# Optimization experiments

Measured on AMD Instinct MI355X. Metric: run time of the kernel, lower is better.

Reference implementation:

```python
import jax, jax.numpy as jnp
import numpy as np

N, E, D, H, O = 10000, 640000, 128, 256, 1


def setup_inputs() -> dict:
    key = jax.random.key(0)
    ks = jax.random.split(key, 10)
    s = 0.05
    return {
        "x": jax.random.normal(ks[0], (N, D), dtype=jnp.float32),
        "edge_index": jax.random.randint(ks[1], (2, E), 0, N, dtype=jnp.int64),
        # GraphConv (PyG): lin_rel (with bias) applied to sum-aggregated neighbors,
        # lin_root (no bias) applied to self features.
        "W_rel": jax.random.normal(ks[2], (D, D), dtype=jnp.float32) * s,
        "b_rel": jnp.zeros((D,), dtype=jnp.float32),
        "W_root": jax.random.normal(ks[3], (D, D), dtype=jnp.float32) * s,
        # MLP: D -> H -> H -> O, ReLU between layers
        "W1": jax.random.normal(ks[4], (H, D), dtype=jnp.float32) * s,
        "b1": jnp.zeros((H,), dtype=jnp.float32),
        "W2": jax.random.normal(ks[5], (H, H), dtype=jnp.float32) * s,
        "b2": jnp.zeros((H,), dtype=jnp.float32),
        "W3": jax.random.normal(ks[6], (O, H), dtype=jnp.float32) * s,
        "b3": jnp.zeros((O,), dtype=jnp.float32),
    }


def reference(x, edge_index, W_rel, b_rel, W_root, W1, b1, W2, b2, W3, b3):
    src, dst = edge_index[0], edge_index[1]
    # gather source features along edges, scatter-add to destinations
    agg = jax.ops.segment_sum(x[src], dst, num_segments=N)  # [N, D]
    h = agg @ W_rel.T + b_rel + x @ W_root.T                 # GraphConv out [N, D]
    h = jax.nn.relu(h @ W1.T + b1)
    h = jax.nn.relu(h @ W2.T + b2)
    h = h @ W3.T + b3                                        # [N, O]
    return jax.nn.sigmoid(h)
```

## Files before the change

kernel.cpp:

```cpp
#include <hip/hip_runtime.h>
#include <hip/hip_bf16.h>
#include <cmath>

constexpr int N_NODES = 10000;
constexpr int D_IN = 128;
constexpr int H_DIM = 256;

constexpr int NB = 157;
constexpr int BCAP = 8192;
constexpr int EPB_A = 4096;

typedef unsigned short u16;
typedef short bf16x8 __attribute__((ext_vector_type(8)));
typedef float f32x4 __attribute__((ext_vector_type(4)));

__device__ inline u16 f2bf(float f) {
    return __builtin_bit_cast(u16, __float2bfloat16(f));
}
__device__ inline float bf2f(u16 u) {
    unsigned int v = (unsigned int)u << 16;
    return __builtin_bit_cast(float, v);
}

__global__ __launch_bounds__(256)
void binsort_a(const int* __restrict__ ei, int* __restrict__ gcnt,
               int* __restrict__ buckets, int E) {
    __shared__ int lcnt[NB], gbase[NB];
    const int t = threadIdx.x;
    for (int i = t; i < NB; i += 256) lcnt[i] = 0;
    __syncthreads();
    const int e0 = blockIdx.x * EPB_A + t;
    int packed[16], lpos[16], bb[16];
#pragma unroll
    for (int j = 0; j < 16; ++j) {
        int e = e0 + j * 256;
        if (e < E) {
            int s = ei[e], d = ei[E + e];
            int b = d >> 6;
            bb[j] = b;
            packed[j] = ((d & 63) << 16) | s;
            lpos[j] = atomicAdd(&lcnt[b], 1);
        } else bb[j] = -1;
    }
    __syncthreads();
    for (int i = t; i < NB; i += 256)
        gbase[i] = atomicAdd(&gcnt[i], lcnt[i]);
    __syncthreads();
#pragma unroll
    for (int j = 0; j < 16; ++j)
        if (bb[j] >= 0)
            buckets[bb[j] * BCAP + gbase[bb[j]] + lpos[j]] = packed[j];
}

__global__ __launch_bounds__(64)
void bucket_scan(const int* __restrict__ gcnt, int* __restrict__ bbase,
                 int* __restrict__ offsets) {
    const int t = threadIdx.x;
    int v[3], sum = 0;
#pragma unroll
    for (int j = 0; j < 3; ++j) {
        int idx = t * 3 + j;
        int d = (idx < NB) ? gcnt[idx] : 0;
        v[j] = sum;
        sum += d;
    }
    int incl = sum;
#pragma unroll
    for (int off = 1; off < 64; off <<= 1) {
        int o = __shfl_up(incl, off);
        if (t >= off) incl += o;
    }
    int excl = incl - sum;
#pragma unroll
    for (int j = 0; j < 3; ++j) {
        int idx = t * 3 + j;
        if (idx < NB) bbase[idx] = excl + v[j];
    }
    if (t == 63) offsets[N_NODES] = incl;
}

__global__ __launch_bounds__(256)
void binsort_b(const int* __restrict__ gcnt, const int* __restrict__ bbase,
               const int* __restrict__ buckets, int* __restrict__ sorted_src,
               int* __restrict__ offsets) {
    __shared__ int edges[BCAP];
    __shared__ int deg[64], cur[64];
    const int b = blockIdx.x, t = threadIdx.x;
    int cnt = gcnt[b]; if (cnt > BCAP) cnt = BCAP;
    const int base = bbase[b];
    if (t < 64) deg[t] = 0;
    __syncthreads();
    for (int i = t; i < cnt; i += 256) {
        int p = buckets[b * BCAP + i];
        edges[i] = p;
        atomicAdd(&deg[p >> 16], 1);
    }
    __syncthreads();
    if (t < 64) {
        int d = deg[t];
        int incl = d;
#pragma unroll
        for (int off = 1; off < 64; off <<= 1) {
            int o = __shfl_up(incl, off);
            if (t >= off) incl += o;
        }
        int excl = incl - d;
        cur[t] = excl;
        int node = b * 64 + t;
        if (node < N_NODES) offsets[node] = base + excl;
    }
    __syncthreads();
    for (int i = t; i < cnt; i += 256) {
        int p = edges[i];
        int pos = atomicAdd(&cur[p >> 16], 1);
        sorted_src[base + pos] = p & 0xffff;
    }
}

__global__ __launch_bounds__(256)
void gather_sum_kernel(const float* __restrict__ x,
                       const int* __restrict__ offsets,
                       const int* __restrict__ sorted_src,
                       u16* __restrict__ A0, int M) {
    int wid = (blockIdx.x * blockDim.x + threadIdx.x) >> 6;
    if (wid >= M) return;
    int lane = threadIdx.x & 63;
    int c = (lane & 31) * 4;
    int r = lane >> 5;
    int beg = offsets[wid], end = offsets[wid + 1];
    int half = (end - beg + 1) >> 1;
    int i = r ? beg + half : beg;
    const int i1 = r ? end : beg + half;
    float4 a0 = {0, 0, 0, 0}, a1 = {0, 0, 0, 0}, a2 = {0, 0, 0, 0}, a3 = {0, 0, 0, 0};
    for (; i + 4 <= i1; i += 4) {
        int s0 = sorted_src[i + 0], s1 = sorted_src[i + 1];
        int s2 = sorted_src[i + 2], s3 = sorted_src[i + 3];
        const float4 v0 = *reinterpret_cast<const float4*>(x + (size_t)s0 * D_IN + c);
        const float4 v1 = *reinterpret_cast<const float4*>(x + (size_t)s1 * D_IN + c);
        const float4 v2 = *reinterpret_cast<const float4*>(x + (size_t)s2 * D_IN + c);
        const float4 v3 = *reinterpret_cast<const float4*>(x + (size_t)s3 * D_IN + c);
        a0.x += v0.x; a0.y += v0.y; a0.z += v0.z; a0.w += v0.w;
        a1.x += v1.x; a1.y += v1.y; a1.z += v1.z; a1.w += v1.w;
        a2.x += v2.x; a2.y += v2.y; a2.z += v2.z; a2.w += v2.w;
        a3.x += v3.x; a3.y += v3.y; a3.z += v3.z; a3.w += v3.w;
    }
    for (; i < i1; ++i) {
        int s = sorted_src[i];
        const float4 v = *reinterpret_cast<const float4*>(x + (size_t)s * D_IN + c);
        a0.x += v.x; a0.y += v.y; a0.z += v.z; a0.w += v.w;
    }
    a0.x += a1.x + a2.x + a3.x;
    a0.y += a1.y + a2.y + a3.y;
    a0.z += a1.z + a2.z + a3.z;
    a0.w += a1.w + a2.w + a3.w;
    a0.x += __shfl_xor(a0.x, 32);
    a0.y += __shfl_xor(a0.y, 32);
    a0.z += __shfl_xor(a0.z, 32);
    a0.w += __shfl_xor(a0.w, 32);
    if (r == 0) {
        ushort4 o;
        o.x = f2bf(a0.x); o.y = f2bf(a0.y); o.z = f2bf(a0.z); o.w = f2bf(a0.w);
        *reinterpret_cast<ushort4*>(A0 + (size_t)wid * 256 + c) = o;
    }
}

__global__ __launch_bounds__(256)
void cast_x_kernel(const float* __restrict__ x, u16* __restrict__ A0, int total4) {
    int idx = blockIdx.x * blockDim.x + threadIdx.x;
    if (idx >= total4) return;
    int row = idx >> 5;
    int c = (idx & 31) * 4;
    float4 v = *reinterpret_cast<const float4*>(x + (size_t)row * D_IN + c);
    ushort4 o;
    o.x = f2bf(v.x); o.y = f2bf(v.y); o.z = f2bf(v.z); o.w = f2bf(v.w);
    *reinterpret_cast<ushort4*>(A0 + (size_t)row * 256 + 128 + c) = o;
}

__global__ __launch_bounds__(256)
void cast_w_kernel(const float* __restrict__ W_rel, const float* __restrict__ W_root,
                   const float* __restrict__ W1, const float* __restrict__ W2,
                   u16* __restrict__ Wcat, u16* __restrict__ W1b, u16* __restrict__ W2b) {
    int idx4 = (blockIdx.x * blockDim.x + threadIdx.x) * 4;
    const float* src;
    u16* dst;
    if (idx4 < 32768) {
        int n = idx4 >> 8, k = idx4 & 255;
        src = (k < 128) ? W_rel + n * 128 + k : W_root + n * 128 + (k - 128);
        dst = Wcat + idx4;
    } else if (idx4 < 65536) {
        src = W1 + (idx4 - 32768);
        dst = W1b + (idx4 - 32768);
    } else {
        src = W2 + (idx4 - 65536);
        dst = W2b + (idx4 - 65536);
    }
    float4 v = *reinterpret_cast<const float4*>(src);
    ushort4 o;
    o.x = f2bf(v.x); o.y = f2bf(v.y); o.z = f2bf(v.z); o.w = f2bf(v.w);
    *reinterpret_cast<ushort4*>(dst) = o;
}

template <int ACT>
__global__ __launch_bounds__(256)
void mfma_gemm(const u16* __restrict__ A, const u16* __restrict__ W,
               const float* __restrict__ bias, u16* __restrict__ C,
               int M, int N, int K) {
    constexpr int LDT = 80;
    __shared__ short As[64 * LDT];
    __shared__ short Ws[64 * LDT];
    const int t = threadIdx.x;
    const int m0 = blockIdx.y * 64;
    const int n0 = blockIdx.x * 64;
    const int w = t >> 6, lane = t & 63;
    const int wr = w >> 1, wc = w & 1;
    const int m_lane = lane & 15, q = lane >> 4;
    f32x4 acc[2][2] = {};
    for (int k0 = 0; k0 < K; k0 += 64) {
        __syncthreads();
#pragma unroll
        for (int L = 0; L < 2; ++L) {
            int idx = t + 256 * L;
            int row = idx >> 3;
            int kc = (idx & 7) * 8;
            int ar = m0 + row; if (ar >= M) ar = M - 1;
            bf16x8 av = *reinterpret_cast<const bf16x8*>(A + (size_t)ar * K + k0 + kc);
            bf16x8 wv = *reinterpret_cast<const bf16x8*>(W + (size_t)(n0 + row) * K + k0 + kc);
            *reinterpret_cast<bf16x8*>(&As[row * LDT + kc]) = av;
            *reinterpret_cast<bf16x8*>(&Ws[row * LDT + kc]) = wv;
        }
        __syncthreads();
#pragma unroll
        for (int kk = 0; kk < 64; kk += 32) {
            const int koff = kk + q * 8;
            bf16x8 af[2], bf[2];
#pragma unroll
            for (int i = 0; i < 2; ++i)
                af[i] = *reinterpret_cast<const bf16x8*>(
                    &As[(wr * 32 + i * 16 + m_lane) * LDT + koff]);
#pragma unroll
            for (int j = 0; j < 2; ++j)
                bf[j] = *reinterpret_cast<const bf16x8*>(
                    &Ws[(wc * 32 + j * 16 + m_lane) * LDT + koff]);
#pragma unroll
            for (int i = 0; i < 2; ++i)
#pragma unroll
                for (int j = 0; j < 2; ++j)
                    acc[i][j] = __builtin_amdgcn_mfma_f32_16x16x32_bf16(
                        af[i], bf[j], acc[i][j], 0, 0, 0);
        }
    }
#pragma unroll
    for (int i = 0; i < 2; ++i)
#pragma unroll
        for (int j = 0; j < 2; ++j) {
            int col = n0 + wc * 32 + j * 16 + m_lane;
            float b = bias[col];
#pragma unroll
            for (int r = 0; r < 4; ++r) {
                int row = m0 + wr * 32 + i * 16 + q * 4 + r;
                if (row >= M) continue;
                float v = acc[i][j][r] + b;
                if (ACT == 1) v = fmaxf(v, 0.f);
                C[(size_t)row * N + col] = f2bf(v);
            }
        }
}

__global__ __launch_bounds__(256)
void head_kernel(const u16* __restrict__ h2, const float* __restrict__ W3,
                 const float* __restrict__ b3, float* __restrict__ out, int M) {
    int wave = threadIdx.x >> 6;
    int lane = threadIdx.x & 63;
    int n = blockIdx.x * 4 + wave;
    if (n >= M) return;
    ushort4 hu = *reinterpret_cast<const ushort4*>(h2 + (size_t)n * H_DIM + lane * 4);
    float4 w = *reinterpret_cast<const float4*>(W3 + lane * 4);
    float dot = bf2f(hu.x) * w.x + bf2f(hu.y) * w.y + bf2f(hu.z) * w.z + bf2f(hu.w) * w.w;
#pragma unroll
    for (int off = 32; off > 0; off >>= 1) dot += __shfl_down(dot, off);
    if (lane == 0) {
        float v = dot + b3[0];
        out[n] = 1.0f / (1.0f + expf(-v));
    }
}

extern "C" void kernel_launch(void* const* d_in, const int* in_sizes, int n_in,
                              void* d_out, int out_size, void* d_ws, size_t ws_size,
                              hipStream_t stream) {
    const float* x      = (const float*)d_in[0];
    const int*   ei     = (const int*)d_in[1];
    const float* W_rel  = (const float*)d_in[2];
    const float* b_rel  = (const float*)d_in[3];
    const float* W_root = (const float*)d_in[4];
    const float* W1     = (const float*)d_in[5];
    const float* b1     = (const float*)d_in[6];
    const float* W2     = (const float*)d_in[7];
    const float* b2     = (const float*)d_in[8];
    const float* W3     = (const float*)d_in[9];
    const float* b3     = (const float*)d_in[10];
    float* out = (float*)d_out;
    const int E = in_sizes[1] / 2;

    char* p = (char*)d_ws;
    auto carve = [&](size_t bytes) { char* r = p; p += (bytes + 63) & ~size_t(63); return r; };
    u16* A0   = (u16*)carve((size_t)N_NODES * 256 * 2);
    u16* h0   = (u16*)carve((size_t)N_NODES * 128 * 2);
    u16* h1   = (u16*)carve((size_t)N_NODES * 256 * 2);
    u16* h2   = (u16*)carve((size_t)N_NODES * 256 * 2);
    u16* Wcat = (u16*)carve(128 * 256 * 2);
    u16* W1b  = (u16*)carve(256 * 128 * 2);
    u16* W2b  = (u16*)carve(256 * 256 * 2);
    int* offsets    = (int*)carve((N_NODES + 4) * 4);
    int* gcnt       = (int*)carve(NB * 4);
    int* bbase      = (int*)carve(NB * 4);
    int* buckets    = (int*)carve((size_t)NB * BCAP * 4);
    int* sorted_src = (int*)carve((size_t)E * 4);

    hipMemsetAsync(gcnt, 0, NB * sizeof(int), stream);
    binsort_a<<<(E + EPB_A - 1) / EPB_A, 256, 0, stream>>>(ei, gcnt, buckets, E);
    bucket_scan<<<1, 64, 0, stream>>>(gcnt, bbase, offsets);
    binsort_b<<<NB, 256, 0, stream>>>(gcnt, bbase, buckets, sorted_src, offsets);
    gather_sum_kernel<<<(N_NODES * 64 + 255) / 256, 256, 0, stream>>>(
        x, offsets, sorted_src, A0, N_NODES);
    cast_x_kernel<<<(N_NODES * 32 + 255) / 256, 256, 0, stream>>>(x, A0, N_NODES * 32);
    cast_w_kernel<<<131072 / 4 / 256, 256, 0, stream>>>(W_rel, W_root, W1, W2,
                                                        Wcat, W1b, W2b);
    {
        dim3 g(128 / 64, (N_NODES + 63) / 64);
        mfma_gemm<0><<<g, 256, 0, stream>>>(A0, Wcat, b_rel, h0, N_NODES, 128, 256);
    }
    {
        dim3 g(256 / 64, (N_NODES + 63) / 64);
        mfma_gemm<1><<<g, 256, 0, stream>>>(h0, W1b, b1, h1, N_NODES, 256, 128);
    }
    {
        dim3 g(256 / 64, (N_NODES + 63) / 64);
        mfma_gemm<1><<<g, 256, 0, stream>>>(h1, W2b, b2, h2, N_NODES, 256, 256);
    }
    head_kernel<<<(N_NODES + 3) / 4, 256, 0, stream>>>(h2, W3, b3, out, N_NODES);
}
```

Baseline: 155.1 us.

## Fuse MLP GEMMs and head into one kernel, merge prep and scan launches

Replaces the three separate MFMA GEMM launches and the head kernel with a single fused kernel that keeps each 64-row tile's intermediates in shared memory. It streams weights straight from global memory and folds the final W3 dot product and sigmoid into the epilogue. It also merges the x/weight casts and the gcnt zeroing into one prep kernel, and moves the bucket scan into binsort_b. The neighbor gather now reads a bf16 copy of x, halving gather bytes at a small precision cost. Together these cut launch count and intermediate global traffic, at the risk of lower occupancy from large shared memory and uncached weight reads.

```diff
diff --git a/kernel.cpp b/kernel.cpp
--- a/kernel.cpp
+++ b/kernel.cpp
@@ -20,6 +20,48 @@
 __device__ inline float bf2f(u16 u) {
     unsigned int v = (unsigned int)u << 16;
     return __builtin_bit_cast(float, v);
+}
+
+constexpr int PREP_XB = 1250, PREP_WB = 128;
+__global__ __launch_bounds__(256)
+void prep_kernel(const float* __restrict__ x,
+                 const float* __restrict__ W_rel, const float* __restrict__ W_root,
+                 const float* __restrict__ W1, const float* __restrict__ W2,
+                 u16* __restrict__ x_bf, u16* __restrict__ A0,
+                 u16* __restrict__ Wcat, u16* __restrict__ W1b, u16* __restrict__ W2b,
+                 int* __restrict__ gcnt) {
+    const int bid = blockIdx.x, t = threadIdx.x;
+    if (bid < PREP_XB) {
+        int idx = bid * 256 + t;
+        if (idx >= N_NODES * 32) return;
+        int row = idx >> 5, c = (idx & 31) * 4;
+        float4 v = *reinterpret_cast<const float4*>(x + (size_t)row * D_IN + c);
+        ushort4 o;
+        o.x = f2bf(v.x); o.y = f2bf(v.y); o.z = f2bf(v.z); o.w = f2bf(v.w);
+        *reinterpret_cast<ushort4*>(x_bf + (size_t)row * D_IN + c) = o;
+        *reinterpret_cast<ushort4*>(A0 + (size_t)row * 256 + 128 + c) = o;
+    } else if (bid < PREP_XB + PREP_WB) {
+        int idx4 = ((bid - PREP_XB) * 256 + t) * 4;
+        const float* src;
+        u16* dst;
+        if (idx4 < 32768) {
+            int n = idx4 >> 8, k = idx4 & 255;
+            src = (k < 128) ? W_rel + n * 128 + k : W_root + n * 128 + (k - 128);
+            dst = Wcat + idx4;
+        } else if (idx4 < 65536) {
+            src = W1 + (idx4 - 32768);
+            dst = W1b + (idx4 - 32768);
+        } else {
+            src = W2 + (idx4 - 65536);
+            dst = W2b + (idx4 - 65536);
+        }
+        float4 v = *reinterpret_cast<const float4*>(src);
+        ushort4 o;
+        o.x = f2bf(v.x); o.y = f2bf(v.y); o.z = f2bf(v.z); o.w = f2bf(v.w);
+        *reinterpret_cast<ushort4*>(dst) = o;
+    } else {
+        if (t < NB) gcnt[t] = 0;
+    }
 }
 
 __global__ __launch_bounds__(256)
@@ -52,44 +94,38 @@
             buckets[bb[j] * BCAP + gbase[bb[j]] + lpos[j]] = packed[j];
 }
 
-__global__ __launch_bounds__(64)
-void bucket_scan(const int* __restrict__ gcnt, int* __restrict__ bbase,
-                 int* __restrict__ offsets) {
-    const int t = threadIdx.x;
-    int v[3], sum = 0;
-#pragma unroll
-    for (int j = 0; j < 3; ++j) {
-        int idx = t * 3 + j;
-        int d = (idx < NB) ? gcnt[idx] : 0;
-        v[j] = sum;
-        sum += d;
-    }
-    int incl = sum;
-#pragma unroll
-    for (int off = 1; off < 64; off <<= 1) {
-        int o = __shfl_up(incl, off);
-        if (t >= off) incl += o;
-    }
-    int excl = incl - sum;
-#pragma unroll
-    for (int j = 0; j < 3; ++j) {
-        int idx = t * 3 + j;
-        if (idx < NB) bbase[idx] = excl + v[j];
-    }
-    if (t == 63) offsets[N_NODES] = incl;
-}
-
-__global__ __launch_bounds__(256)
-void binsort_b(const int* __restrict__ gcnt, const int* __restrict__ bbase,
-               const int* __restrict__ buckets, int* __restrict__ sorted_src,
-               int* __restrict__ offsets) {
+__global__ __launch_bounds__(256)
+void binsort_b(const int* __restrict__ gcnt, const int* __restrict__ buckets,
+               int* __restrict__ sorted_src, int* __restrict__ offsets, int E) {
     __shared__ int edges[BCAP];
     __shared__ int deg[64], cur[64];
+    __shared__ int sbase;
     const int b = blockIdx.x, t = threadIdx.x;
+    if (t < 64) {
+        int v[3], sum = 0;
+#pragma unroll
+        for (int j = 0; j < 3; ++j) {
+            int idx = t * 3 + j;
+            int d = (idx < NB) ? gcnt[idx] : 0;
+            v[j] = sum;
+            sum += d;
+        }
+        int incl = sum;
+#pragma unroll
+        for (int off = 1; off < 64; off <<= 1) {
+            int o = __shfl_up(incl, off);
+            if (t >= off) incl += o;
+        }
+        int excl = incl - sum;
+#pragma unroll
+        for (int j = 0; j < 3; ++j)
+            if (t * 3 + j == b) sbase = excl + v[j];
+    }
+    if (t < 64) deg[t] = 0;
+    if (b == 0 && t == 0) offsets[N_NODES] = E;
+    __syncthreads();
+    const int base = sbase;
     int cnt = gcnt[b]; if (cnt > BCAP) cnt = BCAP;
-    const int base = bbase[b];
-    if (t < 64) deg[t] = 0;
-    __syncthreads();
     for (int i = t; i < cnt; i += 256) {
         int p = buckets[b * BCAP + i];
         edges[i] = p;
@@ -118,7 +154,7 @@
 }
 
 __global__ __launch_bounds__(256)
-void gather_sum_kernel(const float* __restrict__ x,
+void gather_sum_kernel(const u16* __restrict__ x_bf,
                        const int* __restrict__ offsets,
                        const int* __restrict__ sorted_src,
                        u16* __restrict__ A0, int M) {
@@ -135,19 +171,19 @@
     for (; i + 4 <= i1; i += 4) {
         int s0 = sorted_src[i + 0], s1 = sorted_src[i + 1];
         int s2 = sorted_src[i + 2], s3 = sorted_src[i + 3];
-        const float4 v0 = *reinterpret_cast<const float4*>(x + (size_t)s0 * D_IN + c);
-        const float4 v1 = *reinterpret_cast<const float4*>(x + (size_t)s1 * D_IN + c);
-        const float4 v2 = *reinterpret_cast<const float4*>(x + (size_t)s2 * D_IN + c);
-        const float4 v3 = *reinterpret_cast<const float4*>(x + (size_t)s3 * D_IN + c);
-        a0.x += v0.x; a0.y += v0.y; a0.z += v0.z; a0.w += v0.w;
-        a1.x += v1.x; a1.y += v1.y; a1.z += v1.z; a1.w += v1.w;
-        a2.x += v2.x; a2.y += v2.y; a2.z += v2.z; a2.w += v2.w;
-        a3.x += v3.x; a3.y += v3.y; a3.z += v3.z; a3.w += v3.w;
+        ushort4 v0 = *reinterpret_cast<const ushort4*>(x_bf + (size_t)s0 * D_IN + c);
+        ushort4 v1 = *reinterpret_cast<const ushort4*>(x_bf + (size_t)s1 * D_IN + c);
+        ushort4 v2 = *reinterpret_cast<const ushort4*>(x_bf + (size_t)s2 * D_IN + c);
+        ushort4 v3 = *reinterpret_cast<const ushort4*>(x_bf + (size_t)s3 * D_IN + c);
+        a0.x += bf2f(v0.x); a0.y += bf2f(v0.y); a0.z += bf2f(v0.z); a0.w += bf2f(v0.w);
+        a1.x += bf2f(v1.x); a1.y += bf2f(v1.y); a1.z += bf2f(v1.z); a1.w += bf2f(v1.w);
+        a2.x += bf2f(v2.x); a2.y += bf2f(v2.y); a2.z += bf2f(v2.z); a2.w += bf2f(v2.w);
+        a3.x += bf2f(v3.x); a3.y += bf2f(v3.y); a3.z += bf2f(v3.z); a3.w += bf2f(v3.w);
     }
     for (; i < i1; ++i) {
         int s = sorted_src[i];
-        const float4 v = *reinterpret_cast<const float4*>(x + (size_t)s * D_IN + c);
-        a0.x += v.x; a0.y += v.y; a0.z += v.z; a0.w += v.w;
+        ushort4 v = *reinterpret_cast<const ushort4*>(x_bf + (size_t)s * D_IN + c);
+        a0.x += bf2f(v.x); a0.y += bf2f(v.y); a0.z += bf2f(v.z); a0.w += bf2f(v.w);
     }
     a0.x += a1.x + a2.x + a3.x;
     a0.y += a1.y + a2.y + a3.y;
@@ -165,122 +201,145 @@
 }
 
 __global__ __launch_bounds__(256)
-void cast_x_kernel(const float* __restrict__ x, u16* __restrict__ A0, int total4) {
-    int idx = blockIdx.x * blockDim.x + threadIdx.x;
-    if (idx >= total4) return;
-    int row = idx >> 5;
-    int c = (idx & 31) * 4;
-    float4 v = *reinterpret_cast<const float4*>(x + (size_t)row * D_IN + c);
-    ushort4 o;
-    o.x = f2bf(v.x); o.y = f2bf(v.y); o.z = f2bf(v.z); o.w = f2bf(v.w);
-    *reinterpret_cast<ushort4*>(A0 + (size_t)row * 256 + 128 + c) = o;
-}
-
-__global__ __launch_bounds__(256)
-void cast_w_kernel(const float* __restrict__ W_rel, const float* __restrict__ W_root,
-                   const float* __restrict__ W1, const float* __restrict__ W2,
-                   u16* __restrict__ Wcat, u16* __restrict__ W1b, u16* __restrict__ W2b) {
-    int idx4 = (blockIdx.x * blockDim.x + threadIdx.x) * 4;
-    const float* src;
-    u16* dst;
-    if (idx4 < 32768) {
-        int n = idx4 >> 8, k = idx4 & 255;
-        src = (k < 128) ? W_rel + n * 128 + k : W_root + n * 128 + (k - 128);
-        dst = Wcat + idx4;
-    } else if (idx4 < 65536) {
-        src = W1 + (idx4 - 32768);
-        dst = W1b + (idx4 - 32768);
-    } else {
-        src = W2 + (idx4 - 65536);
-        dst = W2b + (idx4 - 65536);
-    }
-    float4 v = *reinterpret_cast<const float4*>(src);
-    ushort4 o;
-    o.x = f2bf(v.x); o.y = f2bf(v.y); o.z = f2bf(v.z); o.w = f2bf(v.w);
-    *reinterpret_cast<ushort4*>(dst) = o;
-}
-
-template <int ACT>
-__global__ __launch_bounds__(256)
-void mfma_gemm(const u16* __restrict__ A, const u16* __restrict__ W,
-               const float* __restrict__ bias, u16* __restrict__ C,
-               int M, int N, int K) {
-    constexpr int LDT = 80;
-    __shared__ short As[64 * LDT];
-    __shared__ short Ws[64 * LDT];
-    const int t = threadIdx.x;
-    const int m0 = blockIdx.y * 64;
-    const int n0 = blockIdx.x * 64;
+void fused_mlp(const u16* __restrict__ A0, const u16* __restrict__ Wcat,
+               const u16* __restrict__ W1b, const u16* __restrict__ W2b,
+               const float* __restrict__ b_rel, const float* __restrict__ b1,
+               const float* __restrict__ b2, const float* __restrict__ W3,
+               const float* __restrict__ b3, float* __restrict__ out, int M) {
+    __shared__ u16 sm[25600];
+    __shared__ float part[64][2];
+    u16* bufA  = sm;
+    u16* bufH0 = sm + 16896;
+    const int t = threadIdx.x, b = blockIdx.x;
     const int w = t >> 6, lane = t & 63;
-    const int wr = w >> 1, wc = w & 1;
-    const int m_lane = lane & 15, q = lane >> 4;
-    f32x4 acc[2][2] = {};
-    for (int k0 = 0; k0 < K; k0 += 64) {
-        __syncthreads();
-#pragma unroll
-        for (int L = 0; L < 2; ++L) {
-            int idx = t + 256 * L;
-            int row = idx >> 3;
-            int kc = (idx & 7) * 8;
-            int ar = m0 + row; if (ar >= M) ar = M - 1;
-            bf16x8 av = *reinterpret_cast<const bf16x8*>(A + (size_t)ar * K + k0 + kc);
-            bf16x8 wv = *reinterpret_cast<const bf16x8*>(W + (size_t)(n0 + row) * K + k0 + kc);
-            *reinterpret_cast<bf16x8*>(&As[row * LDT + kc]) = av;
-            *reinterpret_cast<bf16x8*>(&Ws[row * LDT + kc]) = wv;
-        }
-        __syncthreads();
-#pragma unroll
-        for (int kk = 0; kk < 64; kk += 32) {
-            const int koff = kk + q * 8;
-            bf16x8 af[2], bf[2];
+    const int wm = w >> 1, wn = w & 1;
+    const int l16 = lane & 15, q = lane >> 4;
+    const int r0 = b * 64;
+
+    for (int idx = t; idx < 2048; idx += 256) {
+        int row = idx >> 5, kc = (idx & 31) * 8;
+        int gr = r0 + row; if (gr >= M) gr = M - 1;
+        bf16x8 v = *reinterpret_cast<const bf16x8*>(A0 + (size_t)gr * 256 + kc);
+        *reinterpret_cast<bf16x8*>(bufA + row * 264 + kc) = v;
+    }
+    __syncthreads();
+
+    {
+        f32x4 acc[2][4] = {};
+#pragma unroll
+        for (int k0 = 0; k0 < 256; k0 += 32) {
+            bf16x8 af[2];
 #pragma unroll
             for (int i = 0; i < 2; ++i)
                 af[i] = *reinterpret_cast<const bf16x8*>(
-                    &As[(wr * 32 + i * 16 + m_lane) * LDT + koff]);
-#pragma unroll
-            for (int j = 0; j < 2; ++j)
-                bf[j] = *reinterpret_cast<const bf16x8*>(
-                    &Ws[(wc * 32 + j * 16 + m_lane) * LDT + koff]);
-#pragma unroll
-            for (int i = 0; i < 2; ++i)
-#pragma unroll
-                for (int j = 0; j < 2; ++j)
-                    acc[i][j] = __builtin_amdgcn_mfma_f32_16x16x32_bf16(
-                        af[i], bf[j], acc[i][j], 0, 0, 0);
-        }
-    }
-#pragma unroll
-    for (int i = 0; i < 2; ++i)
-#pragma unroll
-        for (int j = 0; j < 2; ++j) {
-            int col = n0 + wc * 32 + j * 16 + m_lane;
-            float b = bias[col];
-#pragma unroll
-            for (int r = 0; r < 4; ++r) {
-                int row = m0 + wr * 32 + i * 16 + q * 4 + r;
-                if (row >= M) continue;
-                float v = acc[i][j][r] + b;
-                if (ACT == 1) v = fmaxf(v, 0.f);
-                C[(size_t)row * N + col] = f2bf(v);
-            }
-        }
-}
-
-__global__ __launch_bounds__(256)
-void head_kernel(const u16* __restrict__ h2, const float* __restrict__ W3,
-                 const float* __restrict__ b3, float* __restrict__ out, int M) {
-    int wave = threadIdx.x >> 6;
-    int lane = threadIdx.x & 63;
-    int n = blockIdx.x * 4 + wave;
-    if (n >= M) return;
-    ushort4 hu = *reinterpret_cast<const ushort4*>(h2 + (size_t)n * H_DIM + lane * 4);
-    float4 w = *reinterpret_cast<const float4*>(W3 + lane * 4);
-    float dot = bf2f(hu.x) * w.x + bf2f(hu.y) * w.y + bf2f(hu.z) * w.z + bf2f(hu.w) * w.w;
-#pragma unroll
-    for (int off = 32; off > 0; off >>= 1) dot += __shfl_down(dot, off);
-    if (lane == 0) {
-        float v = dot + b3[0];
-        out[n] = 1.0f / (1.0f + expf(-v));
+                    bufA + (wm * 32 + i * 16 + l16) * 264 + k0 + q * 8);
+#pragma unroll
+            for (int jj = 0; jj < 4; ++jj) {
+                int col = wn * 64 + jj * 16 + l16;
+                bf16x8 bfv = *reinterpret_cast<const bf16x8*>(
+                    Wcat + (size_t)col * 256 + k0 + q * 8);
+                acc[0][jj] = __builtin_amdgcn_mfma_f32_16x16x32_bf16(af[0], bfv, acc[0][jj], 0, 0, 0);
+                acc[1][jj] = __builtin_amdgcn_mfma_f32_16x16x32_bf16(af[1], bfv, acc[1][jj], 0, 0, 0);
+            }
+        }
+#pragma unroll
+        for (int i = 0; i < 2; ++i)
+#pragma unroll
+            for (int jj = 0; jj < 4; ++jj) {
+                int col = wn * 64 + jj * 16 + l16;
+                float bb = b_rel[col];
+#pragma unroll
+                for (int r = 0; r < 4; ++r) {
+                    int row = wm * 32 + i * 16 + q * 4 + r;
+                    bufH0[row * 136 + col] = f2bf(acc[i][jj][r] + bb);
+                }
+            }
+    }
+    __syncthreads();
+
+    {
+        f32x4 acc[2][8] = {};
+#pragma unroll
+        for (int k0 = 0; k0 < 128; k0 += 32) {
+            bf16x8 af[2];
+#pragma unroll
+            for (int i = 0; i < 2; ++i)
+                af[i] = *reinterpret_cast<const bf16x8*>(
+                    bufH0 + (wm * 32 + i * 16 + l16) * 136 + k0 + q * 8);
+#pragma unroll
+            for (int jj = 0; jj < 8; ++jj) {
+                int col = wn * 128 + jj * 16 + l16;
+                bf16x8 bfv = *reinterpret_cast<const bf16x8*>(
+                    W1b + (size_t)col * 128 + k0 + q * 8);
+                acc[0][jj] = __builtin_amdgcn_mfma_f32_16x16x32_bf16(af[0], bfv, acc[0][jj], 0, 0, 0);
+                acc[1][jj] = __builtin_amdgcn_mfma_f32_16x16x32_bf16(af[1], bfv, acc[1][jj], 0, 0, 0);
+            }
+        }
+#pragma unroll
+        for (int i = 0; i < 2; ++i)
+#pragma unroll
+            for (int jj = 0; jj < 8; ++jj) {
+                int col = wn * 128 + jj * 16 + l16;
+                float bb = b1[col];
+#pragma unroll
+                for (int r = 0; r < 4; ++r) {
+                    int row = wm * 32 + i * 16 + q * 4 + r;
+                    bufA[row * 264 + col] = f2bf(fmaxf(acc[i][jj][r] + bb, 0.f));
+                }
+            }
+    }
+    __syncthreads();
+
+    {
+        f32x4 acc[2][8] = {};
+#pragma unroll
+        for (int k0 = 0; k0 < 256; k0 += 32) {
+            bf16x8 af[2];
+#pragma unroll
+            for (int i = 0; i < 2; ++i)
+                af[i] = *reinterpret_cast<const bf16x8*>(
+                    bufA + (wm * 32 + i * 16 + l16) * 264 + k0 + q * 8);
+#pragma unroll
+            for (int jj = 0; jj < 8; ++jj) {
+                int col = wn * 128 + jj * 16 + l16;
+                bf16x8 bfv = *reinterpret_cast<const bf16x8*>(
+                    W2b + (size_t)col * 256 + k0 + q * 8);
+                acc[0][jj] = __builtin_amdgcn_mfma_f32_16x16x32_bf16(af[0], bfv, acc[0][jj], 0, 0, 0);
+                acc[1][jj] = __builtin_amdgcn_mfma_f32_16x16x32_bf16(af[1], bfv, acc[1][jj], 0, 0, 0);
+            }
+        }
+        float s[2][4] = {};
+#pragma unroll
+        for (int jj = 0; jj < 8; ++jj) {
+            int col = wn * 128 + jj * 16 + l16;
+            float bb = b2[col], ww = W3[col];
+#pragma unroll
+            for (int i = 0; i < 2; ++i)
+#pragma unroll
+                for (int r = 0; r < 4; ++r)
+                    s[i][r] = fmaf(fmaxf(acc[i][jj][r] + bb, 0.f), ww, s[i][r]);
+        }
+#pragma unroll
+        for (int off = 1; off < 16; off <<= 1)
+#pragma unroll
+            for (int i = 0; i < 2; ++i)
+#pragma unroll
+                for (int r = 0; r < 4; ++r)
+                    s[i][r] += __shfl_xor(s[i][r], off);
+        if (l16 == 0)
+#pragma unroll
+            for (int i = 0; i < 2; ++i)
+#pragma unroll
+                for (int r = 0; r < 4; ++r)
+                    part[wm * 32 + i * 16 + q * 4 + r][wn] = s[i][r];
+    }
+    __syncthreads();
+    if (t < 64) {
+        int node = r0 + t;
+        if (node < M) {
+            float v = part[t][0] + part[t][1] + b3[0];
+            out[node] = 1.0f / (1.0f + expf(-v));
+        }
     }
 }
 
@@ -304,38 +363,21 @@
     char* p = (char*)d_ws;
     auto carve = [&](size_t bytes) { char* r = p; p += (bytes + 63) & ~size_t(63); return r; };
     u16* A0   = (u16*)carve((size_t)N_NODES * 256 * 2);
-    u16* h0   = (u16*)carve((size_t)N_NODES * 128 * 2);
-    u16* h1   = (u16*)carve((size_t)N_NODES * 256 * 2);
-    u16* h2   = (u16*)carve((size_t)N_NODES * 256 * 2);
+    u16* x_bf = (u16*)carve((size_t)N_NODES * D_IN * 2);
     u16* Wcat = (u16*)carve(128 * 256 * 2);
     u16* W1b  = (u16*)carve(256 * 128 * 2);
     u16* W2b  = (u16*)carve(256 * 256 * 2);
     int* offsets    = (int*)carve((N_NODES + 4) * 4);
     int* gcnt       = (int*)carve(NB * 4);
-    int* bbase      = (int*)carve(NB * 4);
     int* buckets    = (int*)carve((size_t)NB * BCAP * 4);
     int* sorted_src = (int*)carve((size_t)E * 4);
 
-    hipMemsetAsync(gcnt, 0, NB * sizeof(int), stream);
+    prep_kernel<<<PREP_XB + PREP_WB + 1, 256, 0, stream>>>(
+        x, W_rel, W_root, W1, W2, x_bf, A0, Wcat, W1b, W2b, gcnt);
     binsort_a<<<(E + EPB_A - 1) / EPB_A, 256, 0, stream>>>(ei, gcnt, buckets, E);
-    bucket_scan<<<1, 64, 0, stream>>>(gcnt, bbase, offsets);
-    binsort_b<<<NB, 256, 0, stream>>>(gcnt, bbase, buckets, sorted_src, offsets);
+    binsort_b<<<NB, 256, 0, stream>>>(gcnt, buckets, sorted_src, offsets, E);
     gather_sum_kernel<<<(N_NODES * 64 + 255) / 256, 256, 0, stream>>>(
-        x, offsets, sorted_src, A0, N_NODES);
-    cast_x_kernel<<<(N_NODES * 32 + 255) / 256, 256, 0, stream>>>(x, A0, N_NODES * 32);
-    cast_w_kernel<<<131072 / 4 / 256, 256, 0, stream>>>(W_rel, W_root, W1, W2,
-                                                        Wcat, W1b, W2b);
-    {
-        dim3 g(128 / 64, (N_NODES + 63) / 64);
-        mfma_gemm<0><<<g, 256, 0, stream>>>(A0, Wcat, b_rel, h0, N_NODES, 128, 256);
-    }
-    {
-        dim3 g(256 / 64, (N_NODES + 63) / 64);
-        mfma_gemm<1><<<g, 256, 0, stream>>>(h0, W1b, b1, h1, N_NODES, 256, 128);
-    }
-    {
-        dim3 g(256 / 64, (N_NODES + 63) / 64);
-        mfma_gemm<1><<<g, 256, 0, stream>>>(h1, W2b, b2, h2, N_NODES, 256, 256);
-    }
-    head_kernel<<<(N_NODES + 3) / 4, 256, 0, stream>>>(h2, W3, b3, out, N_NODES);
-}
+        x_bf, offsets, sorted_src, A0, N_NODES);
+    fused_mlp<<<(N_NODES + 63) / 64, 256, 0, stream>>>(
+        A0, Wcat, W1b, W2b, b_rel, b1, b2, W3, b3, out, N_NODES);
+}
```

Result: no change. 152.8 us (-1.5%).
